# Kernel optimization log

Measured on AMD Instinct MI355X. Metric: run time of the kernel, lower is better.

## Reference

```python
import jax, jax.numpy as jnp
import numpy as np

OUT_H = OUT_W = 7          # cfg.output_size
S = 2                      # fixed samples per bin (static replacement for data-dependent ceil(stride))
G = OUT_H * S              # sampling grid side = 14
SCALES = (0.25, 0.125, 0.0625, 0.03125)   # cfg.pooler_scales for P2..P5
SIZES = (256, 128, 64, 32)                # per-level feature H=W


def _roi_align(feat_p2, feat_p3, feat_p4, feat_p5, proposals):
    # Pad all levels to the largest spatial size and stack -> [4, C, 256, 256].
    # Index clamping below never reads past each level's valid region.
    Hmax = SIZES[0]
    levels = []
    for f, s in zip((feat_p2, feat_p3, feat_p4, feat_p5), SIZES):
        levels.append(jnp.pad(f[0], ((0, 0), (0, Hmax - s), (0, Hmax - s))))
    F = jnp.stack(levels)                      # [4, C, 256, 256]

    N = proposals.shape[0]
    pw = proposals[:, 2] - proposals[:, 0]
    ph = proposals[:, 3] - proposals[:, 1]
    # FPN level assignment: floor(2 + log2(sqrt(area)/224)), clamped to [0,3]
    lvl = jnp.clip(jnp.floor(2.0 + jnp.log2(jnp.sqrt(pw * ph) / 224.0)), 0, 3).astype(jnp.int32)

    sc = jnp.asarray(SCALES, proposals.dtype)[lvl]          # [N]
    box = proposals * sc[:, None]                           # scale to feature coords
    bx1, by1, bx2, by2 = box[:, 0], box[:, 1], box[:, 2], box[:, 3]

    w_stride = (bx2 - bx1) / OUT_W
    h_stride = (by2 - by1) / OUT_H
    w_unit = w_stride / S
    h_unit = h_stride / S

    idx = jnp.arange(G, dtype=proposals.dtype) + 0.5        # sample centers
    xs = bx1[:, None] + idx[None, :] * w_unit[:, None]      # [N, G]
    ys = by1[:, None] + idx[None, :] * h_unit[:, None]      # [N, G]
    x = jnp.broadcast_to(xs[:, None, :], (N, G, G))         # [N, Gy, Gx]
    y = jnp.broadcast_to(ys[:, :, None], (N, G, G))

    # Per-level valid extent for clamping (mirrors feature.shape clamps)
    size_l = jnp.asarray(SIZES, jnp.int32)[lvl][:, None, None]   # [N,1,1]

    x0 = jnp.clip(jnp.floor(x).astype(jnp.int32), 0, size_l - 1)
    x1i = jnp.clip(jnp.floor(x).astype(jnp.int32) + 1, 0, size_l - 1)
    y0 = jnp.clip(jnp.floor(y).astype(jnp.int32), 0, size_l - 1)
    y1i = jnp.clip(jnp.floor(y).astype(jnp.int32) + 1, 0, size_l - 1)

    # Weights use the CLAMPED indices, matching the in-place clamp_ in the original.
    x0f, x1f = x0.astype(x.dtype), x1i.astype(x.dtype)
    y0f, y1f = y0.astype(y.dtype), y1i.astype(y.dtype)
    wa = (x1f - x) * (y1f - y)
    wb = (x1f - x) * (y - y0f)
    wc = (x - x0f) * (y1f - y)
    wd = (x - x0f) * (y - y0f)

    lv = jnp.broadcast_to(lvl[:, None, None], (N, G, G))
    la = F[lv, :, y0, x0]      # [N, G, G, C] gathers (irregular access hotspot)
    lb = F[lv, :, y1i, x0]
    lc = F[lv, :, y0, x1i]
    ld = F[lv, :, y1i, x1i]

    interp = (wa[..., None] * la + wb[..., None] * lb
              + wc[..., None] * lc + wd[..., None] * ld)   # [N, G, G, C]

    C = F.shape[1]
    # Adaptive max pool (7,7): exact SxS blocks since G = 7*S
    pooled = interp.reshape(N, OUT_H, S, OUT_W, S, C).max(axis=(2, 4))  # [N,7,7,C]
    return jnp.transpose(pooled, (0, 3, 1, 2))                          # [N,C,7,7]


def setup_inputs() -> dict:
    key = jax.random.key(0)
    k0, k1, k2, k3, k4 = jax.random.split(key, 5)
    C = 256
    feat_p2 = jax.random.normal(k0, (1, C, 256, 256), jnp.float32)
    feat_p3 = jax.random.normal(k1, (1, C, 128, 128), jnp.float32)
    feat_p4 = jax.random.normal(k2, (1, C, 64, 64), jnp.float32)
    feat_p5 = jax.random.normal(k3, (1, C, 32, 32), jnp.float32)
    N = 512
    u = jax.random.uniform(k4, (N, 4), jnp.float32)
    x1 = u[:, 0] * 700.0
    y1 = u[:, 1] * 700.0
    w = 32.0 + u[:, 2] * 292.0
    h = 32.0 + u[:, 3] * 292.0
    proposals = jnp.stack([x1, y1, x1 + w, y1 + h], axis=1)  # [N,4] image coords
    return {"feat_p2": feat_p2, "feat_p3": feat_p3, "feat_p4": feat_p4,
            "feat_p5": feat_p5, "proposals": proposals}


def reference(feat_p2, feat_p3, feat_p4, feat_p5, proposals):
    return _roi_align(feat_p2, feat_p3, feat_p4, feat_p5, proposals)
```

## Files before the change

kernel.cpp:

```cpp
#include <hip/hip_runtime.h>
#include <hip/hip_bf16.h>
#include <math.h>

#define C_CH 256

__global__ __launch_bounds__(256) void transpose_all(
    const float* __restrict__ f0, const float* __restrict__ f1,
    const float* __restrict__ f2, const float* __restrict__ f3,
    __hip_bfloat16* __restrict__ tf) {
  __shared__ float tile[64][65];
  const int b = blockIdx.x;
  const float* src;
  int S, lg;
  size_t dstoff;
  int sb;
  if (b < 4096) {
    src = f0; S = 65536; lg = 10; dstoff = 0;     sb = b;
  } else if (b < 5120) {
    src = f1; S = 16384; lg = 8;  dstoff = 65536; sb = b - 4096;
  } else if (b < 5376) {
    src = f2; S = 4096;  lg = 6;  dstoff = 81920; sb = b - 5120;
  } else {
    src = f3; S = 1024;  lg = 4;  dstoff = 86016; sb = b - 5376;
  }
  const int nsp_m1 = (1 << lg) - 1;
  const int s0 = (sb & nsp_m1) * 64;
  const int c0 = (sb >> lg) * 64;

  const int t = threadIdx.x;
  {
    const int cl = t >> 4;
    const int sp4 = (t & 15) * 4;
    #pragma unroll
    for (int j = 0; j < 4; ++j) {
      const int c = cl + 16 * j;
      const float4 v = *(const float4*)(src + (size_t)(c0 + c) * S + s0 + sp4);
      tile[c][sp4 + 0] = v.x;
      tile[c][sp4 + 1] = v.y;
      tile[c][sp4 + 2] = v.z;
      tile[c][sp4 + 3] = v.w;
    }
  }
  __syncthreads();
  {
    const int spl = t >> 4;
    const int c4 = (t & 15) * 4;
    __hip_bfloat16* dst = tf + (dstoff + (size_t)s0) * C_CH + c0;
    #pragma unroll
    for (int j = 0; j < 4; ++j) {
      const int sp = spl + 16 * j;
      union { ushort4 u; __hip_bfloat16 h[4]; } p;
      p.h[0] = __float2bfloat16(tile[c4 + 0][sp]);
      p.h[1] = __float2bfloat16(tile[c4 + 1][sp]);
      p.h[2] = __float2bfloat16(tile[c4 + 2][sp]);
      p.h[3] = __float2bfloat16(tile[c4 + 3][sp]);
      *(ushort4*)(dst + (size_t)sp * C_CH + c4) = p.u;
    }
  }
}

__device__ __forceinline__ float bfu(unsigned short s) {
  union { unsigned u; float f; } v;
  v.u = (unsigned)s << 16;
  return v.f;
}

__global__ __launch_bounds__(64) void roi_bf16(
    const unsigned short* __restrict__ tf,
    const float* __restrict__ proposals, float* __restrict__ out) {
  __shared__ int xo0[14], xo1[14];
  __shared__ float wxa[14], wxb[14];
  __shared__ int yo_s[4];
  __shared__ float wy_s[4];

  const int n = blockIdx.x;
  const int oh = blockIdx.y;
  const int lane = threadIdx.x;

  const float px1 = proposals[n * 4 + 0];
  const float py1 = proposals[n * 4 + 1];
  const float px2 = proposals[n * 4 + 2];
  const float py2 = proposals[n * 4 + 3];
  float lt = 2.0f + log2f(sqrtf((px2 - px1) * (py2 - py1)) / 224.0f);
  int lvl = (int)floorf(lt);
  lvl = lvl < 0 ? 0 : (lvl > 3 ? 3 : lvl);

  const float scales[4] = {0.25f, 0.125f, 0.0625f, 0.03125f};
  const int sizes[4] = {256, 128, 64, 32};
  const int offs[4] = {0, 65536, 81920, 86016};
  const float sc = scales[lvl];
  const int sz = sizes[lvl];

  const float bx1 = px1 * sc, by1 = py1 * sc;
  const float w_unit = ((px2 - px1) * sc / 7.0f) * 0.5f;
  const float h_unit = ((py2 - py1) * sc / 7.0f) * 0.5f;

  if (lane < 14) {
    const int i = lane;
    float x = bx1 + ((float)i + 0.5f) * w_unit;
    int xf = (int)floorf(x);
    int x0 = min(max(xf, 0), sz - 1);
    int x1 = min(max(xf + 1, 0), sz - 1);
    wxa[i] = (float)x1 - x;
    wxb[i] = x - (float)x0;
    xo0[i] = x0 * C_CH;
    xo1[i] = x1 * C_CH;
  } else if (lane >= 32 && lane < 34) {
    const int j = lane - 32;
    float y = by1 + ((float)(2 * oh + j) + 0.5f) * h_unit;
    int yf = (int)floorf(y);
    int y0 = min(max(yf, 0), sz - 1);
    int y1 = min(max(yf + 1, 0), sz - 1);
    yo_s[j * 2 + 0] = y0 * sz * C_CH;
    yo_s[j * 2 + 1] = y1 * sz * C_CH;
    wy_s[j * 2 + 0] = (float)y1 - y;
    wy_s[j * 2 + 1] = y - (float)y0;
  }
  __syncthreads();

  const unsigned short* base = tf + (size_t)offs[lvl] * C_CH + lane * 4;
  const unsigned short* r00 = base + yo_s[0];
  const unsigned short* r01 = base + yo_s[1];
  const unsigned short* r10 = base + yo_s[2];
  const unsigned short* r11 = base + yo_s[3];
  const float wy0a = wy_s[0], wy0b = wy_s[1];
  const float wy1a = wy_s[2], wy1b = wy_s[3];

  float mm[7][4];
  #pragma unroll
  for (int ow = 0; ow < 7; ++ow)
    #pragma unroll
    for (int k = 0; k < 4; ++k) mm[ow][k] = -INFINITY;

  #pragma unroll 2
  for (int gx = 0; gx < 14; ++gx) {
    const int xa = xo0[gx], xb = xo1[gx];
    const ushort4 A0 = *(const ushort4*)(r00 + xa);
    const ushort4 A1 = *(const ushort4*)(r00 + xb);
    const ushort4 B0 = *(const ushort4*)(r01 + xa);
    const ushort4 B1 = *(const ushort4*)(r01 + xb);
    const ushort4 C0 = *(const ushort4*)(r10 + xa);
    const ushort4 C1 = *(const ushort4*)(r10 + xb);
    const ushort4 D0 = *(const ushort4*)(r11 + xa);
    const ushort4 D1 = *(const ushort4*)(r11 + xb);
    const float fa = wxa[gx], fb = wxb[gx];
    const int ow = gx >> 1;
    const unsigned short* a0 = (const unsigned short*)&A0;
    const unsigned short* a1 = (const unsigned short*)&A1;
    const unsigned short* b0 = (const unsigned short*)&B0;
    const unsigned short* b1 = (const unsigned short*)&B1;
    const unsigned short* c0 = (const unsigned short*)&C0;
    const unsigned short* c1 = (const unsigned short*)&C1;
    const unsigned short* d0 = (const unsigned short*)&D0;
    const unsigned short* d1 = (const unsigned short*)&D1;
    #pragma unroll
    for (int k = 0; k < 4; ++k) {
      const float h00 = fa * bfu(a0[k]) + fb * bfu(a1[k]);
      const float h01 = fa * bfu(b0[k]) + fb * bfu(b1[k]);
      const float va = wy0a * h00 + wy0b * h01;
      const float h10 = fa * bfu(c0[k]) + fb * bfu(c1[k]);
      const float h11 = fa * bfu(d0[k]) + fb * bfu(d1[k]);
      const float vb = wy1a * h10 + wy1b * h11;
      mm[ow][k] = fmaxf(mm[ow][k], fmaxf(va, vb));
    }
  }

  float* ob = out + ((size_t)n * C_CH + lane * 4) * 49 + oh * 7;
  #pragma unroll
  for (int k = 0; k < 4; ++k)
    #pragma unroll
    for (int ow = 0; ow < 7; ++ow) ob[k * 49 + ow] = mm[ow][k];
}

__global__ __launch_bounds__(64) void roi_fallback(
    const float* __restrict__ f0, const float* __restrict__ f1,
    const float* __restrict__ f2, const float* __restrict__ f3,
    const float* __restrict__ proposals, float* __restrict__ out) {
  __shared__ int xo0[14], xo1[14], yo0[14], yo1[14];
  __shared__ float wxa[14], wxb[14], wya[14], wyb[14];
  const int n = blockIdx.x;
  const int cblk = blockIdx.y;
  const int lane = threadIdx.x;
  const int c = cblk * 64 + lane;
  const float px1 = proposals[n * 4 + 0];
  const float py1 = proposals[n * 4 + 1];
  const float px2 = proposals[n * 4 + 2];
  const float py2 = proposals[n * 4 + 3];
  float lt = 2.0f + log2f(sqrtf((px2 - px1) * (py2 - py1)) / 224.0f);
  int lvl = (int)floorf(lt);
  lvl = lvl < 0 ? 0 : (lvl > 3 ? 3 : lvl);
  const float scales[4] = {0.25f, 0.125f, 0.0625f, 0.03125f};
  const int sizes[4] = {256, 128, 64, 32};
  const float sc = scales[lvl];
  const int sz = sizes[lvl];
  const float bx1 = px1 * sc, by1 = py1 * sc;
  const float w_unit = ((px2 - px1) * sc / 7.0f) * 0.5f;
  const float h_unit = ((py2 - py1) * sc / 7.0f) * 0.5f;
  if (lane < 14) {
    float x = bx1 + ((float)lane + 0.5f) * w_unit;
    int xf = (int)floorf(x);
    int x0 = min(max(xf, 0), sz - 1);
    int x1 = min(max(xf + 1, 0), sz - 1);
    wxa[lane] = (float)x1 - x;
    wxb[lane] = x - (float)x0;
    xo0[lane] = x0;
    xo1[lane] = x1;
  } else if (lane >= 32 && lane < 46) {
    const int i = lane - 32;
    float y = by1 + ((float)i + 0.5f) * h_unit;
    int yf = (int)floorf(y);
    int y0 = min(max(yf, 0), sz - 1);
    int y1 = min(max(yf + 1, 0), sz - 1);
    wya[i] = (float)y1 - y;
    wyb[i] = y - (float)y0;
    yo0[i] = y0 * sz;
    yo1[i] = y1 * sz;
  }
  __syncthreads();
  const float* fl = (lvl == 0) ? f0 : (lvl == 1) ? f1 : (lvl == 2) ? f2 : f3;
  const float* base = fl + (size_t)c * sz * sz;
  for (int oh = 0; oh < 7; ++oh) {
    float mm[7];
    #pragma unroll
    for (int ow = 0; ow < 7; ++ow) mm[ow] = -INFINITY;
    #pragma unroll
    for (int sy = 0; sy < 2; ++sy) {
      const int gy = oh * 2 + sy;
      const float* r0 = base + yo0[gy];
      const float* r1 = base + yo1[gy];
      const float wy0 = wya[gy], wy1 = wyb[gy];
      #pragma unroll
      for (int gx = 0; gx < 14; ++gx) {
        float v = wy0 * (wxa[gx] * r0[xo0[gx]] + wxb[gx] * r0[xo1[gx]]) +
                  wy1 * (wxa[gx] * r1[xo0[gx]] + wxb[gx] * r1[xo1[gx]]);
        mm[gx >> 1] = fmaxf(mm[gx >> 1], v);
      }
    }
    #pragma unroll
    for (int ow = 0; ow < 7; ++ow)
      out[((size_t)n * C_CH + c) * 49 + oh * 7 + ow] = mm[ow];
  }
}

extern "C" void kernel_launch(void* const* d_in, const int* in_sizes, int n_in,
                              void* d_out, int out_size, void* d_ws,
                              size_t ws_size, hipStream_t stream) {
  const float* f0 = (const float*)d_in[0];
  const float* f1 = (const float*)d_in[1];
  const float* f2 = (const float*)d_in[2];
  const float* f3 = (const float*)d_in[3];
  const float* props = (const float*)d_in[4];
  float* out = (float*)d_out;
  const int N = in_sizes[4] / 4;

  const size_t needed = (size_t)87040 * C_CH * sizeof(__hip_bfloat16);
  if (ws_size >= needed) {
    __hip_bfloat16* tf = (__hip_bfloat16*)d_ws;
    transpose_all<<<5440, 256, 0, stream>>>(f0, f1, f2, f3, tf);
    roi_bf16<<<dim3(N, 7), 64, 0, stream>>>((const unsigned short*)tf, props,
                                            out);
  } else {
    roi_fallback<<<dim3(N, 4), 64, 0, stream>>>(f0, f1, f2, f3, props, out);
  }
}
```

Baseline: 156.7 us.

## Merge per-row ROI blocks into one block and stage output in LDS for coalesced stores

The ROI kernel now launches one 512-thread block per proposal, with 7 active wavefronts each computing one output row instead of 7 separate 64-thread blocks. Results are staged in a padded shared-memory buffer and then written to the NCHW output with fully coalesced contiguous stores, replacing the strided per-thread scalar stores. The gx loop is fully unrolled. The cost is about 51KB of LDS per block, an idle eighth wavefront, and two barriers, all of which can lower occupancy.

```diff
diff --git a/kernel.cpp b/kernel.cpp
--- a/kernel.cpp
+++ b/kernel.cpp
@@ -65,17 +65,19 @@
   return v.f;
 }
 
-__global__ __launch_bounds__(64) void roi_bf16(
+#define OPAD 260
+
+__global__ __launch_bounds__(512) void roi_bf16(
     const unsigned short* __restrict__ tf,
     const float* __restrict__ proposals, float* __restrict__ out) {
-  __shared__ int xo0[14], xo1[14];
-  __shared__ float wxa[14], wxb[14];
-  __shared__ int yo_s[4];
-  __shared__ float wy_s[4];
+  __shared__ int xo0[14], xo1[14], yo0[14], yo1[14];
+  __shared__ float wxa[14], wxb[14], wya[14], wyb[14];
+  __shared__ float obuf[49 * OPAD];
 
   const int n = blockIdx.x;
-  const int oh = blockIdx.y;
-  const int lane = threadIdx.x;
+  const int t = threadIdx.x;
+  const int lane = t & 63;
+  const int w = t >> 6;
 
   const float px1 = proposals[n * 4 + 0];
   const float py1 = proposals[n * 4 + 1];
@@ -95,8 +97,8 @@
   const float w_unit = ((px2 - px1) * sc / 7.0f) * 0.5f;
   const float h_unit = ((py2 - py1) * sc / 7.0f) * 0.5f;
 
-  if (lane < 14) {
-    const int i = lane;
+  if (t < 14) {
+    const int i = t;
     float x = bx1 + ((float)i + 0.5f) * w_unit;
     int xf = (int)floorf(x);
     int x0 = min(max(xf, 0), sz - 1);
@@ -105,71 +107,83 @@
     wxb[i] = x - (float)x0;
     xo0[i] = x0 * C_CH;
     xo1[i] = x1 * C_CH;
-  } else if (lane >= 32 && lane < 34) {
-    const int j = lane - 32;
-    float y = by1 + ((float)(2 * oh + j) + 0.5f) * h_unit;
+  } else if (t >= 64 && t < 78) {
+    const int i = t - 64;
+    float y = by1 + ((float)i + 0.5f) * h_unit;
     int yf = (int)floorf(y);
     int y0 = min(max(yf, 0), sz - 1);
     int y1 = min(max(yf + 1, 0), sz - 1);
-    yo_s[j * 2 + 0] = y0 * sz * C_CH;
-    yo_s[j * 2 + 1] = y1 * sz * C_CH;
-    wy_s[j * 2 + 0] = (float)y1 - y;
-    wy_s[j * 2 + 1] = y - (float)y0;
-  }
-  __syncthreads();
-
-  const unsigned short* base = tf + (size_t)offs[lvl] * C_CH + lane * 4;
-  const unsigned short* r00 = base + yo_s[0];
-  const unsigned short* r01 = base + yo_s[1];
-  const unsigned short* r10 = base + yo_s[2];
-  const unsigned short* r11 = base + yo_s[3];
-  const float wy0a = wy_s[0], wy0b = wy_s[1];
-  const float wy1a = wy_s[2], wy1b = wy_s[3];
-
-  float mm[7][4];
-  #pragma unroll
-  for (int ow = 0; ow < 7; ++ow)
-    #pragma unroll
-    for (int k = 0; k < 4; ++k) mm[ow][k] = -INFINITY;
-
-  #pragma unroll 2
-  for (int gx = 0; gx < 14; ++gx) {
-    const int xa = xo0[gx], xb = xo1[gx];
-    const ushort4 A0 = *(const ushort4*)(r00 + xa);
-    const ushort4 A1 = *(const ushort4*)(r00 + xb);
-    const ushort4 B0 = *(const ushort4*)(r01 + xa);
-    const ushort4 B1 = *(const ushort4*)(r01 + xb);
-    const ushort4 C0 = *(const ushort4*)(r10 + xa);
-    const ushort4 C1 = *(const ushort4*)(r10 + xb);
-    const ushort4 D0 = *(const ushort4*)(r11 + xa);
-    const ushort4 D1 = *(const ushort4*)(r11 + xb);
-    const float fa = wxa[gx], fb = wxb[gx];
-    const int ow = gx >> 1;
-    const unsigned short* a0 = (const unsigned short*)&A0;
-    const unsigned short* a1 = (const unsigned short*)&A1;
-    const unsigned short* b0 = (const unsigned short*)&B0;
-    const unsigned short* b1 = (const unsigned short*)&B1;
-    const unsigned short* c0 = (const unsigned short*)&C0;
-    const unsigned short* c1 = (const unsigned short*)&C1;
-    const unsigned short* d0 = (const unsigned short*)&D0;
-    const unsigned short* d1 = (const unsigned short*)&D1;
-    #pragma unroll
-    for (int k = 0; k < 4; ++k) {
-      const float h00 = fa * bfu(a0[k]) + fb * bfu(a1[k]);
-      const float h01 = fa * bfu(b0[k]) + fb * bfu(b1[k]);
-      const float va = wy0a * h00 + wy0b * h01;
-      const float h10 = fa * bfu(c0[k]) + fb * bfu(c1[k]);
-      const float h11 = fa * bfu(d0[k]) + fb * bfu(d1[k]);
-      const float vb = wy1a * h10 + wy1b * h11;
-      mm[ow][k] = fmaxf(mm[ow][k], fmaxf(va, vb));
-    }
-  }
-
-  float* ob = out + ((size_t)n * C_CH + lane * 4) * 49 + oh * 7;
-  #pragma unroll
-  for (int k = 0; k < 4; ++k)
-    #pragma unroll
-    for (int ow = 0; ow < 7; ++ow) ob[k * 49 + ow] = mm[ow][k];
+    wya[i] = (float)y1 - y;
+    wyb[i] = y - (float)y0;
+    yo0[i] = y0 * sz * C_CH;
+    yo1[i] = y1 * sz * C_CH;
+  }
+  __syncthreads();
+
+  if (w < 7) {
+    const int oh = w;
+    const int gy0 = 2 * oh, gy1 = 2 * oh + 1;
+    const unsigned short* base = tf + (size_t)offs[lvl] * C_CH + lane * 4;
+    const unsigned short* r00 = base + yo0[gy0];
+    const unsigned short* r01 = base + yo1[gy0];
+    const unsigned short* r10 = base + yo0[gy1];
+    const unsigned short* r11 = base + yo1[gy1];
+    const float wy0a = wya[gy0], wy0b = wyb[gy0];
+    const float wy1a = wya[gy1], wy1b = wyb[gy1];
+
+    float mm[7][4];
+    #pragma unroll
+    for (int j = 0; j < 7; ++j)
+      #pragma unroll
+      for (int k = 0; k < 4; ++k) mm[j][k] = -INFINITY;
+
+    #pragma unroll
+    for (int gx = 0; gx < 14; ++gx) {
+      const int xa = xo0[gx], xb = xo1[gx];
+      const ushort4 A0 = *(const ushort4*)(r00 + xa);
+      const ushort4 A1 = *(const ushort4*)(r00 + xb);
+      const ushort4 B0 = *(const ushort4*)(r01 + xa);
+      const ushort4 B1 = *(const ushort4*)(r01 + xb);
+      const ushort4 C0 = *(const ushort4*)(r10 + xa);
+      const ushort4 C1 = *(const ushort4*)(r10 + xb);
+      const ushort4 D0 = *(const ushort4*)(r11 + xa);
+      const ushort4 D1 = *(const ushort4*)(r11 + xb);
+      const float fa = wxa[gx], fb = wxb[gx];
+      const int j = gx >> 1;
+      const unsigned short* a0 = (const unsigned short*)&A0;
+      const unsigned short* a1 = (const unsigned short*)&A1;
+      const unsigned short* b0 = (const unsigned short*)&B0;
+      const unsigned short* b1 = (const unsigned short*)&B1;
+      const unsigned short* c0 = (const unsigned short*)&C0;
+      const unsigned short* c1 = (const unsigned short*)&C1;
+      const unsigned short* d0 = (const unsigned short*)&D0;
+      const unsigned short* d1 = (const unsigned short*)&D1;
+      #pragma unroll
+      for (int k = 0; k < 4; ++k) {
+        const float h00 = fa * bfu(a0[k]) + fb * bfu(a1[k]);
+        const float h01 = fa * bfu(b0[k]) + fb * bfu(b1[k]);
+        const float va = wy0a * h00 + wy0b * h01;
+        const float h10 = fa * bfu(c0[k]) + fb * bfu(c1[k]);
+        const float h11 = fa * bfu(d0[k]) + fb * bfu(d1[k]);
+        const float vb = wy1a * h10 + wy1b * h11;
+        mm[j][k] = fmaxf(mm[j][k], fmaxf(va, vb));
+      }
+    }
+
+    #pragma unroll
+    for (int ow = 0; ow < 7; ++ow) {
+      float4 v = make_float4(mm[ow][0], mm[ow][1], mm[ow][2], mm[ow][3]);
+      *(float4*)&obuf[(oh * 7 + ow) * OPAD + lane * 4] = v;
+    }
+  }
+  __syncthreads();
+
+  float* ob = out + (size_t)n * (C_CH * 49);
+  for (int i = t; i < C_CH * 49; i += 512) {
+    const unsigned c = (unsigned)i / 49u;
+    const unsigned p = (unsigned)i - c * 49u;
+    ob[i] = obuf[p * OPAD + c];
+  }
 }
 
 __global__ __launch_bounds__(64) void roi_fallback(
@@ -257,8 +271,7 @@
   if (ws_size >= needed) {
     __hip_bfloat16* tf = (__hip_bfloat16*)d_ws;
     transpose_all<<<5440, 256, 0, stream>>>(f0, f1, f2, f3, tf);
-    roi_bf16<<<dim3(N, 7), 64, 0, stream>>>((const unsigned short*)tf, props,
-                                            out);
+    roi_bf16<<<N, 512, 0, stream>>>((const unsigned short*)tf, props, out);
   } else {
     roi_fallback<<<dim3(N, 4), 64, 0, stream>>>(f0, f1, f2, f3, props, out);
   }
```

Result: faster. 144.9 us (-7.6%).
